# Performance work log

Measured on AMD Instinct MI355X. Metric: run time of the kernel, lower is better.

The kernel has to match this reference:

```python
import jax, jax.numpy as jnp
import numpy as np

N, NFEAT, NHID, NCLASS, NHEADS = 4096, 512, 64, 128, 8
ALPHA = 0.2
NEG = -9e15


def leaky(x):
    return jnp.where(x > 0, x, ALPHA * x)


def setup_inputs() -> dict:
    key = jax.random.key(0)
    k = jax.random.split(key, 6)
    x = jax.random.normal(k[0], (N, NFEAT), dtype=jnp.float32)
    adj = jax.random.randint(k[1], (N, N), 0, 2, dtype=jnp.int32)
    # per-head params (xavier-ish scale)
    W = jax.random.normal(k[2], (NHEADS, NFEAT, NHID), dtype=jnp.float32) * (1.414 * (2.0 / (NFEAT + NHID)) ** 0.5)
    a = jax.random.normal(k[3], (NHEADS, 2 * NHID), dtype=jnp.float32) * (1.414 * (2.0 / (2 * NHID + 1)) ** 0.5)
    W_out = jax.random.normal(k[4], (NHEADS * NHID, NCLASS), dtype=jnp.float32) * (1.414 * (2.0 / (NHEADS * NHID + NCLASS)) ** 0.5)
    a_out = jax.random.normal(k[5], (2 * NCLASS,), dtype=jnp.float32) * (1.414 * (2.0 / (2 * NCLASS + 1)) ** 0.5)
    return {"x": x, "adj": adj, "W": W, "a": a, "W_out": W_out, "a_out": a_out}


def _gat_layer_multihead(x, adj_mask, W, a):
    # x: [N,F_in], W: [H,F_in,F_out], a: [H,2*F_out]
    h = jnp.einsum('nf,hfo->hno', x, W)           # [H,N,F_out]
    Fo = W.shape[-1]
    a1, a2 = a[:, :Fo], a[:, Fo:]                  # [H,F_out] each
    fi = jnp.einsum('hno,ho->hn', h, a1)           # score contribution of node i
    fj = jnp.einsum('hno,ho->hn', h, a2)
    e = leaky(fi[:, :, None] + fj[:, None, :])     # [H,N,N] == leakyrelu(a . [h_i||h_j])
    e = jnp.where(adj_mask[None], e, NEG)
    att = jax.nn.softmax(e, axis=-1)
    return jnp.einsum('hij,hjo->hio', att, h)      # [H,N,F_out]


def reference(x, adj, W, a, W_out, a_out):
    adj_mask = adj > 0
    # multi-head hidden layer, concat heads (dropout is identity in eval mode)
    hp = _gat_layer_multihead(x, adj_mask, W, a)            # [H,N,NHID]
    xcat = jnp.transpose(hp, (1, 0, 2)).reshape(N, NHEADS * NHID)
    # output attention layer (single head)
    out = _gat_layer_multihead(xcat, adj_mask, W_out[None], a_out[None])[0]  # [N,NCLASS]
    out = jax.nn.elu(out)
    return jax.nn.log_softmax(out, axis=1)
```

## Files before the change

kernel.cpp:

```cpp
#include <hip/hip_runtime.h>
#include <hip/hip_bf16.h>

#define NNODE 4096

typedef __attribute__((ext_vector_type(8))) short bf16x8;
typedef __attribute__((ext_vector_type(4))) float f32x4;
typedef __attribute__((ext_vector_type(8))) unsigned short us8;

__device__ __forceinline__ unsigned short f2bf(float x) {
  __hip_bfloat16 b = __float2bfloat16(x);
  return __builtin_bit_cast(unsigned short, b);
}

__global__ __launch_bounds__(256) void packadj(
    const int* __restrict__ adj, unsigned long long* __restrict__ mask) {
  size_t wid = (size_t)blockIdx.x * 4 + (threadIdx.x >> 6);
  int v = adj[wid * 64 + (threadIdx.x & 63)];
  unsigned long long b = __ballot(v != 0);
  if ((threadIdx.x & 63) == 0) mask[wid] = b;
}

__global__ __launch_bounds__(256) void transpose_bf16(
    const float* __restrict__ src, short* __restrict__ dst, int Nr, int Fsrc) {
  __shared__ float tile[64][68];
  const int t  = threadIdx.x;
  const int n0 = blockIdx.x * 64, o0 = blockIdx.y * 64;
  const int h  = blockIdx.z;
  const float* S = src + ((size_t)h * Nr + n0) * Fsrc + o0;
  short* D = dst + ((size_t)h * Fsrc + o0) * Nr + n0;
  const int r = t >> 2, cs = (t & 3) * 16;
  #pragma unroll
  for (int k2 = 0; k2 < 4; ++k2) {
    float4 v = *(const float4*)&S[(size_t)r * Fsrc + cs + k2 * 4];
    *(float4*)&tile[r][cs + k2 * 4] = v;
  }
  __syncthreads();
  const int o = t >> 2, ns = (t & 3) * 16;
  us8 u0, u1;
  #pragma unroll
  for (int e = 0; e < 8; ++e) u0[e] = f2bf(tile[ns + e][o]);
  #pragma unroll
  for (int e = 0; e < 8; ++e) u1[e] = f2bf(tile[ns + 8 + e][o]);
  *(us8*)&D[(size_t)o * Nr + ns]     = u0;
  *(us8*)&D[(size_t)o * Nr + ns + 8] = u1;
}

__global__ __launch_bounds__(256) void gemm_mfma(
    const float* __restrict__ A, const short* __restrict__ Wt,
    float* __restrict__ C, int M, int K, int Nfull) {
  __shared__ short As[64][72];
  const int t  = threadIdx.x;
  const int lane = t & 63;
  const int w  = t >> 6;
  const int i0 = blockIdx.x * 64;
  const int c0 = blockIdx.y * 64;
  const int h  = blockIdx.z;
  const short* Bh = Wt + ((size_t)h * Nfull + c0) * K;
  float*       Ch = C + (size_t)h * M * Nfull;

  const int R0 = (w >> 1) * 32;
  const int C0 = (w & 1) * 32;
  const int lr = lane & 15;
  const int lk = lane >> 4;

  const int arow = t >> 2;
  const int aseg = (t & 3) * 16;

  f32x4 acc[2][2] = {};

  const short* b00p = &Bh[(size_t)(C0 + lr) * K + lk * 8];
  const short* b10p = &Bh[(size_t)(C0 + 16 + lr) * K + lk * 8];

  bf16x8 bc[4];
  bc[0] = *(const bf16x8*)(b00p);
  bc[1] = *(const bf16x8*)(b10p);
  bc[2] = *(const bf16x8*)(b00p + 32);
  bc[3] = *(const bf16x8*)(b10p + 32);

  for (int k0 = 0; k0 < K; k0 += 64) {
    {
      const float* src = &A[(size_t)(i0 + arow) * K + k0 + aseg];
      float4 v0 = *(const float4*)(src);
      float4 v1 = *(const float4*)(src + 4);
      float4 v2 = *(const float4*)(src + 8);
      float4 v3 = *(const float4*)(src + 12);
      us8 u0, u1;
      u0[0] = f2bf(v0.x); u0[1] = f2bf(v0.y); u0[2] = f2bf(v0.z); u0[3] = f2bf(v0.w);
      u0[4] = f2bf(v1.x); u0[5] = f2bf(v1.y); u0[6] = f2bf(v1.z); u0[7] = f2bf(v1.w);
      u1[0] = f2bf(v2.x); u1[1] = f2bf(v2.y); u1[2] = f2bf(v2.z); u1[3] = f2bf(v2.w);
      u1[4] = f2bf(v3.x); u1[5] = f2bf(v3.y); u1[6] = f2bf(v3.z); u1[7] = f2bf(v3.w);
      *(us8*)&As[arow][aseg]     = u0;
      *(us8*)&As[arow][aseg + 8] = u1;
    }
    bf16x8 bn[4];
    {
      int kn = (k0 + 64 < K) ? (k0 + 64) : k0;
      bn[0] = *(const bf16x8*)(b00p + kn);
      bn[1] = *(const bf16x8*)(b10p + kn);
      bn[2] = *(const bf16x8*)(b00p + kn + 32);
      bn[3] = *(const bf16x8*)(b10p + kn + 32);
    }
    __syncthreads();
    #pragma unroll
    for (int kc = 0; kc < 64; kc += 32) {
      bf16x8 a0 = *(const bf16x8*)&As[R0 + lr][kc + lk * 8];
      bf16x8 a1 = *(const bf16x8*)&As[R0 + 16 + lr][kc + lk * 8];
      bf16x8 b0 = bc[(kc >> 5) * 2 + 0];
      bf16x8 b1 = bc[(kc >> 5) * 2 + 1];
      acc[0][0] = __builtin_amdgcn_mfma_f32_16x16x32_bf16(a0, b0, acc[0][0], 0, 0, 0);
      acc[0][1] = __builtin_amdgcn_mfma_f32_16x16x32_bf16(a0, b1, acc[0][1], 0, 0, 0);
      acc[1][0] = __builtin_amdgcn_mfma_f32_16x16x32_bf16(a1, b0, acc[1][0], 0, 0, 0);
      acc[1][1] = __builtin_amdgcn_mfma_f32_16x16x32_bf16(a1, b1, acc[1][1], 0, 0, 0);
    }
    bc[0] = bn[0]; bc[1] = bn[1]; bc[2] = bn[2]; bc[3] = bn[3];
    __syncthreads();
  }

  #pragma unroll
  for (int fa = 0; fa < 2; ++fa) {
    #pragma unroll
    for (int fb = 0; fb < 2; ++fb) {
      #pragma unroll
      for (int reg = 0; reg < 4; ++reg) {
        int row = R0 + fa * 16 + lk * 4 + reg;
        int col = C0 + fb * 16 + lr;
        Ch[(size_t)(i0 + row) * Nfull + c0 + col] = acc[fa][fb][reg];
      }
    }
  }
}

template<int F>
__global__ __launch_bounds__(256) void wa_kernel(
    const float* __restrict__ W, const float* __restrict__ a,
    float* __restrict__ wa) {
  const int gid  = blockIdx.x * 4 + (threadIdx.x >> 6);
  const int lane = threadIdx.x & 63;
  const int h = gid >> 9;
  const int k = gid & 511;
  const float* wrow = W + ((size_t)h * 512 + k) * F;
  const float* ah = a + h * 2 * F;
  float v1 = 0.f, v2 = 0.f;
  #pragma unroll
  for (int o = lane; o < F; o += 64) {
    float wv = wrow[o];
    v1 += wv * ah[o];
    v2 += wv * ah[F + o];
  }
  #pragma unroll
  for (int off = 32; off; off >>= 1) {
    v1 += __shfl_xor(v1, off);
    v2 += __shfl_xor(v2, off);
  }
  if (lane == 0) {
    wa[((size_t)h * 2 + 0) * 512 + k] = v1;
    wa[((size_t)h * 2 + 1) * 512 + k] = v2;
  }
}

template<int NH>
__global__ __launch_bounds__(256) void fidot_kernel(
    const float* __restrict__ X, const float* __restrict__ wa,
    float* __restrict__ fi, float* __restrict__ fj,
    float* __restrict__ eiP, float* __restrict__ eiN,
    float* __restrict__ ejP, float* __restrict__ ejN) {
  const int gid  = blockIdx.x * 4 + (threadIdx.x >> 6);
  const int lane = threadIdx.x & 63;
  const int h = gid >> 12;
  const int n = gid & 4095;
  const float* xr = X + (size_t)n * 512;
  const float* w1 = wa + (size_t)h * 2 * 512;
  const float* w2 = w1 + 512;
  float v1 = 0.f, v2 = 0.f;
  #pragma unroll
  for (int it = 0; it < 8; ++it) {
    int k = lane + it * 64;
    float xv = xr[k];
    v1 += xv * w1[k];
    v2 += xv * w2[k];
  }
  #pragma unroll
  for (int off = 32; off; off >>= 1) {
    v1 += __shfl_xor(v1, off);
    v2 += __shfl_xor(v2, off);
  }
  if (lane == 0) {
    int idx = h * NNODE + n;
    fi[idx] = v1;
    fj[idx] = v2;
    eiP[idx] = __expf(v1);
    eiN[idx] = __expf(0.2f * v1);
    ejP[idx] = __expf(v2);
    ejN[idx] = __expf(0.2f * v2);
  }
}

template<int OT, int JLEN>
__global__ __launch_bounds__(256) void pv_split(
    const short* __restrict__ hT, const float* __restrict__ fi,
    const float* __restrict__ eiP, const float* __restrict__ eiN,
    const float* __restrict__ fj, const float* __restrict__ ejP,
    const float* __restrict__ ejN, const unsigned long long* __restrict__ mask,
    float* __restrict__ pnum, float* __restrict__ pl, int Fh) {
  __shared__ short pT[64][72];
  __shared__ short hTl[OT][64][72];
  __shared__ float fjL[64], ejPL[64], ejNL[64];
  __shared__ float lred[64][4];

  const int t      = threadIdx.x;
  const int lane   = t & 63;
  const int w      = t >> 6;
  const int i0     = blockIdx.x * 64;
  const int chunk  = blockIdx.y;
  const int nchunk = gridDim.y;
  const int h      = blockIdx.z;
  const int hN     = h * NNODE;
  const short* hTs = hT + (size_t)h * Fh * NNODE;

  const int R0 = (w >> 1) * 32;
  const int C0 = (w & 1) * 32;
  const int lr = lane & 15;
  const int lk = lane >> 4;

  const int ar = t >> 2;
  const int jc = (t & 3) * 16;
  const float thr  = -fi[hN + i0 + ar];
  const float eiPr = eiP[hN + i0 + ar];
  const float eiNr = eiN[hN + i0 + ar];
  const unsigned short* mrow =
      (const unsigned short*)mask + (size_t)(i0 + ar) * (NNODE / 16);

  f32x4 acc[OT][2][2] = {};
  float lsum = 0.0f;

  const int jbase = chunk * JLEN;
  for (int jt = 0; jt < JLEN; jt += 64) {
    const int j0 = jbase + jt;
    {
      const int o = t >> 2, seg = t & 3;
      #pragma unroll
      for (int ot = 0; ot < OT; ++ot) {
        const short* src = hTs + (size_t)(ot * 64 + o) * NNODE + j0 + seg * 16;
        float4 v0 = *(const float4*)(src);
        float4 v1 = *(const float4*)(src + 8);
        *(float4*)&hTl[ot][o][seg * 16]     = v0;
        *(float4*)&hTl[ot][o][seg * 16 + 8] = v1;
      }
    }
    if (t < 64) {
      fjL[t]  = fj[hN + j0 + t];
      ejPL[t] = ejP[hN + j0 + t];
      ejNL[t] = ejN[hN + j0 + t];
    }
    __syncthreads();

    {
      unsigned int mb = mrow[(j0 + jc) >> 4];
      unsigned short pk[16];
      #pragma unroll
      for (int g = 0; g < 4; ++g) {
        float4 f4 = *(const float4*)&fjL[jc + g * 4];
        float4 eP = *(const float4*)&ejPL[jc + g * 4];
        float4 eN = *(const float4*)&ejNL[jc + g * 4];
        float p0 = (f4.x > thr) ? eiPr * eP.x : eiNr * eN.x;
        float p1 = (f4.y > thr) ? eiPr * eP.y : eiNr * eN.y;
        float p2 = (f4.z > thr) ? eiPr * eP.z : eiNr * eN.z;
        float p3 = (f4.w > thr) ? eiPr * eP.w : eiNr * eN.w;
        p0 = (mb & (1u << (4 * g + 0))) ? p0 : 0.f;
        p1 = (mb & (1u << (4 * g + 1))) ? p1 : 0.f;
        p2 = (mb & (1u << (4 * g + 2))) ? p2 : 0.f;
        p3 = (mb & (1u << (4 * g + 3))) ? p3 : 0.f;
        lsum += p0 + p1 + p2 + p3;
        pk[4 * g + 0] = f2bf(p0); pk[4 * g + 1] = f2bf(p1);
        pk[4 * g + 2] = f2bf(p2); pk[4 * g + 3] = f2bf(p3);
      }
      *(us8*)&pT[ar][jc]     = *(const us8*)&pk[0];
      *(us8*)&pT[ar][jc + 8] = *(const us8*)&pk[8];
    }
    __syncthreads();

    #pragma unroll
    for (int kc = 0; kc < 64; kc += 32) {
      bf16x8 a0 = *(const bf16x8*)&pT[R0 + lr][kc + lk * 8];
      bf16x8 a1 = *(const bf16x8*)&pT[R0 + 16 + lr][kc + lk * 8];
      #pragma unroll
      for (int ot = 0; ot < OT; ++ot) {
        bf16x8 b0 = *(const bf16x8*)&hTl[ot][C0 + lr][kc + lk * 8];
        bf16x8 b1 = *(const bf16x8*)&hTl[ot][C0 + 16 + lr][kc + lk * 8];
        acc[ot][0][0] = __builtin_amdgcn_mfma_f32_16x16x32_bf16(a0, b0, acc[ot][0][0], 0, 0, 0);
        acc[ot][0][1] = __builtin_amdgcn_mfma_f32_16x16x32_bf16(a0, b1, acc[ot][0][1], 0, 0, 0);
        acc[ot][1][0] = __builtin_amdgcn_mfma_f32_16x16x32_bf16(a1, b0, acc[ot][1][0], 0, 0, 0);
        acc[ot][1][1] = __builtin_amdgcn_mfma_f32_16x16x32_bf16(a1, b1, acc[ot][1][1], 0, 0, 0);
      }
    }
    __syncthreads();
  }

  lred[ar][t & 3] = lsum;
  __syncthreads();
  if (t < 64)
    pl[(size_t)(h * nchunk + chunk) * NNODE + i0 + t] =
        lred[t][0] + lred[t][1] + lred[t][2] + lred[t][3];

  float* pout = pnum + ((size_t)(h * nchunk + chunk) * NNODE + i0) * (OT * 64);
  #pragma unroll
  for (int ot = 0; ot < OT; ++ot) {
    #pragma unroll
    for (int fa = 0; fa < 2; ++fa) {
      #pragma unroll
      for (int fb = 0; fb < 2; ++fb) {
        #pragma unroll
        for (int reg = 0; reg < 4; ++reg) {
          int row = R0 + fa * 16 + lk * 4 + reg;
          int col = ot * 64 + C0 + fb * 16 + lr;
          pout[(size_t)row * (OT * 64) + col] = acc[ot][fa][fb][reg];
        }
      }
    }
  }
}

template<int NC>
__global__ __launch_bounds__(256) void combine1(
    const float* __restrict__ pnum, const float* __restrict__ pl,
    float* __restrict__ xcat) {
  const int n = blockIdx.x, t = threadIdx.x;
  #pragma unroll
  for (int rep = 0; rep < 2; ++rep) {
    int col = t + rep * 256;
    int h = col >> 6, o = col & 63;
    float s = 0.f, L = 0.f;
    #pragma unroll
    for (int c = 0; c < NC; ++c) {
      s += pnum[((size_t)(h * NC + c) * NNODE + n) * 64 + o];
      L += pl[(size_t)(h * NC + c) * NNODE + n];
    }
    xcat[(size_t)n * 512 + col] = s / L;
  }
}

__global__ __launch_bounds__(128) void combine2_final(
    const float* __restrict__ pnum, const float* __restrict__ pl,
    float* __restrict__ dout) {
  const int n = blockIdx.x, t = threadIdx.x;
  float s = 0.f, L = 0.f;
  #pragma unroll
  for (int c = 0; c < 8; ++c) {
    s += pnum[((size_t)c * NNODE + n) * 128 + t];
    L += pl[(size_t)c * NNODE + n];
  }
  float v = s / L;
  float e = v > 0.f ? v : (__expf(v) - 1.0f);
  float mx = e;
  #pragma unroll
  for (int off = 32; off; off >>= 1) mx = fmaxf(mx, __shfl_xor(mx, off));
  __shared__ float r2[2];
  if ((t & 63) == 0) r2[t >> 6] = mx;
  __syncthreads();
  mx = fmaxf(r2[0], r2[1]);
  float sm = __expf(e - mx);
  #pragma unroll
  for (int off = 32; off; off >>= 1) sm += __shfl_xor(sm, off);
  __shared__ float s2[2];
  if ((t & 63) == 0) s2[t >> 6] = sm;
  __syncthreads();
  float sum = s2[0] + s2[1];
  dout[(size_t)n * 128 + t] = e - mx - __logf(sum);
}

extern "C" void kernel_launch(void* const* d_in, const int* in_sizes, int n_in,
                              void* d_out, int out_size, void* d_ws, size_t ws_size,
                              hipStream_t stream) {
  const float* x     = (const float*)d_in[0];
  const int*   adj   = (const int*)d_in[1];
  const float* W     = (const float*)d_in[2];
  const float* a     = (const float*)d_in[3];
  const float* W_out = (const float*)d_in[4];
  const float* a_out = (const float*)d_in[5];
  float* out = (float*)d_out;

  float* ws = (float*)d_ws;
  unsigned long long* mask = (unsigned long long*)ws;
  float* hbuf = ws + 524288;
  float* xcat = hbuf + 2097152;
  short* hT   = (short*)(xcat + 2097152);
  float* pnum = (float*)(((short*)hT) + 2097152);
  float* pl   = pnum + 4194304;
  short* Wt1  = (short*)(pl + 131072);
  short* Wt2  = Wt1 + 262144;
  float* fi1  = (float*)(Wt2 + 65536);
  float* fj1  = fi1 + 32768;
  float* eiP1 = fj1 + 32768;
  float* eiN1 = eiP1 + 32768;
  float* ejP1 = eiN1 + 32768;
  float* ejN1 = ejP1 + 32768;
  float* fi2  = ejN1 + 32768;
  float* fj2  = fi2 + 4096;
  float* eiP2 = fj2 + 4096;
  float* eiN2 = eiP2 + 4096;
  float* ejP2 = eiN2 + 4096;
  float* ejN2 = ejP2 + 4096;
  float* wa1  = ejN2 + 4096;
  float* wa2  = wa1 + 8192;

  packadj<<<dim3(NNODE * NNODE / 64 / 4), 256, 0, stream>>>(adj, mask);
  transpose_bf16<<<dim3(8, 1, 8), 256, 0, stream>>>(W, Wt1, 512, 64);
  transpose_bf16<<<dim3(8, 2, 1), 256, 0, stream>>>(W_out, Wt2, 512, 128);
  wa_kernel<64><<<dim3(8 * 512 / 4), 256, 0, stream>>>(W, a, wa1);
  wa_kernel<128><<<dim3(512 / 4), 256, 0, stream>>>(W_out, a_out, wa2);

  gemm_mfma<<<dim3(64, 1, 8), 256, 0, stream>>>(x, Wt1, hbuf, 4096, 512, 64);
  transpose_bf16<<<dim3(64, 1, 8), 256, 0, stream>>>(hbuf, hT, 4096, 64);
  fidot_kernel<8><<<dim3(8 * 4096 / 4), 256, 0, stream>>>(x, wa1, fi1, fj1, eiP1, eiN1, ejP1, ejN1);
  pv_split<1, 2048><<<dim3(64, 2, 8), 256, 0, stream>>>(hT, fi1, eiP1, eiN1, fj1, ejP1, ejN1, mask, pnum, pl, 64);
  combine1<2><<<dim3(NNODE), 256, 0, stream>>>(pnum, pl, xcat);

  gemm_mfma<<<dim3(64, 2, 1), 256, 0, stream>>>(xcat, Wt2, hbuf, 4096, 512, 128);
  transpose_bf16<<<dim3(64, 2, 1), 256, 0, stream>>>(hbuf, hT, 4096, 128);
  fidot_kernel<1><<<dim3(4096 / 4), 256, 0, stream>>>(xcat, wa2, fi2, fj2, eiP2, eiN2, ejP2, ejN2);
  pv_split<2, 512><<<dim3(64, 8, 1), 256, 0, stream>>>(hT, fi2, eiP2, eiN2, fj2, ejP2, ejN2, mask, pnum, pl, 128);
  combine2_final<<<dim3(NNODE), 128, 0, stream>>>(pnum, pl, out);
}
```

Measured before the change: 273.2 us.

## Fuse transposes into GEMM epilogue, register-resident P in attention, fuse fidot into combine

The GEMM now writes its output directly as transposed bf16, which removes the separate fp32 hbuf and the transpose kernels. The pv_split kernel builds the attention-probability A-fragment in registers, with each wave owning 16 rows. This drops the pT shared-memory staging and one barrier per tile. fidot for layer 1 handles all 8 heads per node with weights staged in LDS, and the layer-2 fidot is fused into combine1, saving launches and rereads of x/xcat. In exchange there are higher register counts, an uncoalesced 4-element transposed store in the GEMM epilogue, and 32KB of LDS per block in fidot8.

```diff
diff --git a/kernel.cpp b/kernel.cpp
--- a/kernel.cpp
+++ b/kernel.cpp
@@ -5,6 +5,7 @@
 
 typedef __attribute__((ext_vector_type(8))) short bf16x8;
 typedef __attribute__((ext_vector_type(4))) float f32x4;
+typedef __attribute__((ext_vector_type(4))) unsigned short us4;
 typedef __attribute__((ext_vector_type(8))) unsigned short us8;
 
 __device__ __forceinline__ unsigned short f2bf(float x) {
@@ -47,7 +48,7 @@
 
 __global__ __launch_bounds__(256) void gemm_mfma(
     const float* __restrict__ A, const short* __restrict__ Wt,
-    float* __restrict__ C, int M, int K, int Nfull) {
+    short* __restrict__ hTout, int M, int K, int Nfull) {
   __shared__ short As[64][72];
   const int t  = threadIdx.x;
   const int lane = t & 63;
@@ -56,7 +57,7 @@
   const int c0 = blockIdx.y * 64;
   const int h  = blockIdx.z;
   const short* Bh = Wt + ((size_t)h * Nfull + c0) * K;
-  float*       Ch = C + (size_t)h * M * Nfull;
+  short*       Hh = hTout + (size_t)h * Nfull * M;
 
   const int R0 = (w >> 1) * 32;
   const int C0 = (w & 1) * 32;
@@ -120,12 +121,12 @@
   for (int fa = 0; fa < 2; ++fa) {
     #pragma unroll
     for (int fb = 0; fb < 2; ++fb) {
+      int col  = c0 + C0 + fb * 16 + lr;
+      int rowb = i0 + R0 + fa * 16 + lk * 4;
+      us4 pk;
       #pragma unroll
-      for (int reg = 0; reg < 4; ++reg) {
-        int row = R0 + fa * 16 + lk * 4 + reg;
-        int col = C0 + fb * 16 + lr;
-        Ch[(size_t)(i0 + row) * Nfull + c0 + col] = acc[fa][fb][reg];
-      }
+      for (int reg = 0; reg < 4; ++reg) pk[reg] = f2bf(acc[fa][fb][reg]);
+      *(us4*)&Hh[(size_t)col * M + rowb] = pk;
     }
   }
 }
@@ -158,40 +159,41 @@
   }
 }
 
-template<int NH>
-__global__ __launch_bounds__(256) void fidot_kernel(
+__global__ __launch_bounds__(256) void fidot8(
     const float* __restrict__ X, const float* __restrict__ wa,
     float* __restrict__ fi, float* __restrict__ fj,
     float* __restrict__ eiP, float* __restrict__ eiN,
     float* __restrict__ ejP, float* __restrict__ ejN) {
-  const int gid  = blockIdx.x * 4 + (threadIdx.x >> 6);
+  __shared__ float sw[8192];
+  for (int idx = threadIdx.x; idx < 8192; idx += 256) sw[idx] = wa[idx];
+  __syncthreads();
+  const int n    = blockIdx.x * 4 + (threadIdx.x >> 6);
   const int lane = threadIdx.x & 63;
-  const int h = gid >> 12;
-  const int n = gid & 4095;
   const float* xr = X + (size_t)n * 512;
-  const float* w1 = wa + (size_t)h * 2 * 512;
-  const float* w2 = w1 + 512;
-  float v1 = 0.f, v2 = 0.f;
+  float v[16] = {};
   #pragma unroll
   for (int it = 0; it < 8; ++it) {
     int k = lane + it * 64;
     float xv = xr[k];
-    v1 += xv * w1[k];
-    v2 += xv * w2[k];
-  }
-  #pragma unroll
-  for (int off = 32; off; off >>= 1) {
-    v1 += __shfl_xor(v1, off);
-    v2 += __shfl_xor(v2, off);
-  }
+    #pragma unroll
+    for (int hh = 0; hh < 8; ++hh) {
+      v[2 * hh]     += xv * sw[(2 * hh) * 512 + k];
+      v[2 * hh + 1] += xv * sw[(2 * hh + 1) * 512 + k];
+    }
+  }
+  #pragma unroll
+  for (int off = 32; off; off >>= 1)
+    #pragma unroll
+    for (int i = 0; i < 16; ++i) v[i] += __shfl_xor(v[i], off);
   if (lane == 0) {
-    int idx = h * NNODE + n;
-    fi[idx] = v1;
-    fj[idx] = v2;
-    eiP[idx] = __expf(v1);
-    eiN[idx] = __expf(0.2f * v1);
-    ejP[idx] = __expf(v2);
-    ejN[idx] = __expf(0.2f * v2);
+    #pragma unroll
+    for (int hh = 0; hh < 8; ++hh) {
+      int idx = hh * NNODE + n;
+      float f1 = v[2 * hh], f2 = v[2 * hh + 1];
+      fi[idx] = f1;  fj[idx] = f2;
+      eiP[idx] = __expf(f1); eiN[idx] = __expf(0.2f * f1);
+      ejP[idx] = __expf(f2); ejN[idx] = __expf(0.2f * f2);
+    }
   }
 }
 
@@ -202,10 +204,8 @@
     const float* __restrict__ fj, const float* __restrict__ ejP,
     const float* __restrict__ ejN, const unsigned long long* __restrict__ mask,
     float* __restrict__ pnum, float* __restrict__ pl, int Fh) {
-  __shared__ short pT[64][72];
   __shared__ short hTl[OT][64][72];
   __shared__ float fjL[64], ejPL[64], ejNL[64];
-  __shared__ float lred[64][4];
 
   const int t      = threadIdx.x;
   const int lane   = t & 63;
@@ -217,20 +217,15 @@
   const int hN     = h * NNODE;
   const short* hTs = hT + (size_t)h * Fh * NNODE;
 
-  const int R0 = (w >> 1) * 32;
-  const int C0 = (w & 1) * 32;
   const int lr = lane & 15;
   const int lk = lane >> 4;
-
-  const int ar = t >> 2;
-  const int jc = (t & 3) * 16;
-  const float thr  = -fi[hN + i0 + ar];
-  const float eiPr = eiP[hN + i0 + ar];
-  const float eiNr = eiN[hN + i0 + ar];
-  const unsigned short* mrow =
-      (const unsigned short*)mask + (size_t)(i0 + ar) * (NNODE / 16);
-
-  f32x4 acc[OT][2][2] = {};
+  const int arow = i0 + w * 16 + lr;
+  const float thr  = -fi[hN + arow];
+  const float eiPr = eiP[hN + arow];
+  const float eiNr = eiN[hN + arow];
+  const unsigned long long* mrow = mask + (size_t)arow * (NNODE / 64);
+
+  f32x4 acc[OT][4] = {};
   float lsum = 0.0f;
 
   const int jbase = chunk * JLEN;
@@ -254,88 +249,104 @@
     }
     __syncthreads();
 
-    {
-      unsigned int mb = mrow[(j0 + jc) >> 4];
-      unsigned short pk[16];
+    const unsigned long long mw = mrow[j0 >> 6];
+    #pragma unroll
+    for (int kk = 0; kk < 2; ++kk) {
+      const int kc = kk * 32;
+      const int kb = kc + lk * 8;
+      float4 fj0 = *(const float4*)&fjL[kb];
+      float4 fj1 = *(const float4*)&fjL[kb + 4];
+      float4 eP0 = *(const float4*)&ejPL[kb];
+      float4 eP1 = *(const float4*)&ejPL[kb + 4];
+      float4 eN0 = *(const float4*)&ejNL[kb];
+      float4 eN1 = *(const float4*)&ejNL[kb + 4];
+      const unsigned int mb = (unsigned int)(mw >> kb) & 0xFFu;
+      float pv[8];
+      pv[0] = (fj0.x > thr) ? eiPr * eP0.x : eiNr * eN0.x;
+      pv[1] = (fj0.y > thr) ? eiPr * eP0.y : eiNr * eN0.y;
+      pv[2] = (fj0.z > thr) ? eiPr * eP0.z : eiNr * eN0.z;
+      pv[3] = (fj0.w > thr) ? eiPr * eP0.w : eiNr * eN0.w;
+      pv[4] = (fj1.x > thr) ? eiPr * eP1.x : eiNr * eN1.x;
+      pv[5] = (fj1.y > thr) ? eiPr * eP1.y : eiNr * eN1.y;
+      pv[6] = (fj1.z > thr) ? eiPr * eP1.z : eiNr * eN1.z;
+      pv[7] = (fj1.w > thr) ? eiPr * eP1.w : eiNr * eN1.w;
+      us8 af;
       #pragma unroll
-      for (int g = 0; g < 4; ++g) {
-        float4 f4 = *(const float4*)&fjL[jc + g * 4];
-        float4 eP = *(const float4*)&ejPL[jc + g * 4];
-        float4 eN = *(const float4*)&ejNL[jc + g * 4];
-        float p0 = (f4.x > thr) ? eiPr * eP.x : eiNr * eN.x;
-        float p1 = (f4.y > thr) ? eiPr * eP.y : eiNr * eN.y;
-        float p2 = (f4.z > thr) ? eiPr * eP.z : eiNr * eN.z;
-        float p3 = (f4.w > thr) ? eiPr * eP.w : eiNr * eN.w;
-        p0 = (mb & (1u << (4 * g + 0))) ? p0 : 0.f;
-        p1 = (mb & (1u << (4 * g + 1))) ? p1 : 0.f;
-        p2 = (mb & (1u << (4 * g + 2))) ? p2 : 0.f;
-        p3 = (mb & (1u << (4 * g + 3))) ? p3 : 0.f;
-        lsum += p0 + p1 + p2 + p3;
-        pk[4 * g + 0] = f2bf(p0); pk[4 * g + 1] = f2bf(p1);
-        pk[4 * g + 2] = f2bf(p2); pk[4 * g + 3] = f2bf(p3);
+      for (int e = 0; e < 8; ++e) {
+        float p = (mb & (1u << e)) ? pv[e] : 0.0f;
+        lsum += p;
+        af[e] = f2bf(p);
       }
-      *(us8*)&pT[ar][jc]     = *(const us8*)&pk[0];
-      *(us8*)&pT[ar][jc + 8] = *(const us8*)&pk[8];
-    }
-    __syncthreads();
-
-    #pragma unroll
-    for (int kc = 0; kc < 64; kc += 32) {
-      bf16x8 a0 = *(const bf16x8*)&pT[R0 + lr][kc + lk * 8];
-      bf16x8 a1 = *(const bf16x8*)&pT[R0 + 16 + lr][kc + lk * 8];
+      bf16x8 a = __builtin_bit_cast(bf16x8, af);
       #pragma unroll
       for (int ot = 0; ot < OT; ++ot) {
-        bf16x8 b0 = *(const bf16x8*)&hTl[ot][C0 + lr][kc + lk * 8];
-        bf16x8 b1 = *(const bf16x8*)&hTl[ot][C0 + 16 + lr][kc + lk * 8];
-        acc[ot][0][0] = __builtin_amdgcn_mfma_f32_16x16x32_bf16(a0, b0, acc[ot][0][0], 0, 0, 0);
-        acc[ot][0][1] = __builtin_amdgcn_mfma_f32_16x16x32_bf16(a0, b1, acc[ot][0][1], 0, 0, 0);
-        acc[ot][1][0] = __builtin_amdgcn_mfma_f32_16x16x32_bf16(a1, b0, acc[ot][1][0], 0, 0, 0);
-        acc[ot][1][1] = __builtin_amdgcn_mfma_f32_16x16x32_bf16(a1, b1, acc[ot][1][1], 0, 0, 0);
-      }
-    }
-    __syncthreads();
-  }
-
-  lred[ar][t & 3] = lsum;
-  __syncthreads();
-  if (t < 64)
-    pl[(size_t)(h * nchunk + chunk) * NNODE + i0 + t] =
-        lred[t][0] + lred[t][1] + lred[t][2] + lred[t][3];
-
-  float* pout = pnum + ((size_t)(h * nchunk + chunk) * NNODE + i0) * (OT * 64);
-  #pragma unroll
-  for (int ot = 0; ot < OT; ++ot) {
-    #pragma unroll
-    for (int fa = 0; fa < 2; ++fa) {
-      #pragma unroll
-      for (int fb = 0; fb < 2; ++fb) {
         #pragma unroll
-        for (int reg = 0; reg < 4; ++reg) {
-          int row = R0 + fa * 16 + lk * 4 + reg;
-          int col = ot * 64 + C0 + fb * 16 + lr;
-          pout[(size_t)row * (OT * 64) + col] = acc[ot][fa][fb][reg];
+        for (int c = 0; c < 4; ++c) {
+          bf16x8 b = *(const bf16x8*)&hTl[ot][c * 16 + lr][kb];
+          acc[ot][c] = __builtin_amdgcn_mfma_f32_16x16x32_bf16(a, b, acc[ot][c], 0, 0, 0);
         }
       }
     }
-  }
-}
-
-template<int NC>
-__global__ __launch_bounds__(256) void combine1(
+    __syncthreads();
+  }
+
+  lsum += __shfl_xor(lsum, 16);
+  lsum += __shfl_xor(lsum, 32);
+  if (lk == 0)
+    pl[(size_t)(h * nchunk + chunk) * NNODE + arow] = lsum;
+
+  float* pout = pnum + ((size_t)(h * nchunk + chunk) * NNODE + i0) * (OT * 64);
+  #pragma unroll
+  for (int ot = 0; ot < OT; ++ot) {
+    #pragma unroll
+    for (int c = 0; c < 4; ++c) {
+      #pragma unroll
+      for (int reg = 0; reg < 4; ++reg) {
+        int row = w * 16 + lk * 4 + reg;
+        int col = ot * 64 + c * 16 + lr;
+        pout[(size_t)row * (OT * 64) + col] = acc[ot][c][reg];
+      }
+    }
+  }
+}
+
+__global__ __launch_bounds__(256) void combine1_fidot(
     const float* __restrict__ pnum, const float* __restrict__ pl,
-    float* __restrict__ xcat) {
+    const float* __restrict__ wa2, float* __restrict__ xcat,
+    float* __restrict__ fi2, float* __restrict__ fj2,
+    float* __restrict__ eiP2, float* __restrict__ eiN2,
+    float* __restrict__ ejP2, float* __restrict__ ejN2) {
   const int n = blockIdx.x, t = threadIdx.x;
+  float d1 = 0.f, d2 = 0.f;
   #pragma unroll
   for (int rep = 0; rep < 2; ++rep) {
     int col = t + rep * 256;
     int h = col >> 6, o = col & 63;
     float s = 0.f, L = 0.f;
     #pragma unroll
-    for (int c = 0; c < NC; ++c) {
-      s += pnum[((size_t)(h * NC + c) * NNODE + n) * 64 + o];
-      L += pl[(size_t)(h * NC + c) * NNODE + n];
-    }
-    xcat[(size_t)n * 512 + col] = s / L;
+    for (int c = 0; c < 2; ++c) {
+      s += pnum[((size_t)(h * 2 + c) * NNODE + n) * 64 + o];
+      L += pl[(size_t)(h * 2 + c) * NNODE + n];
+    }
+    float xv = s / L;
+    xcat[(size_t)n * 512 + col] = xv;
+    d1 += xv * wa2[col];
+    d2 += xv * wa2[512 + col];
+  }
+  #pragma unroll
+  for (int off = 32; off; off >>= 1) {
+    d1 += __shfl_xor(d1, off);
+    d2 += __shfl_xor(d2, off);
+  }
+  __shared__ float red[2][4];
+  if ((t & 63) == 0) { red[0][t >> 6] = d1; red[1][t >> 6] = d2; }
+  __syncthreads();
+  if (t == 0) {
+    float f1 = red[0][0] + red[0][1] + red[0][2] + red[0][3];
+    float f2 = red[1][0] + red[1][1] + red[1][2] + red[1][3];
+    fi2[n] = f1;  fj2[n] = f2;
+    eiP2[n] = __expf(f1); eiN2[n] = __expf(0.2f * f1);
+    ejP2[n] = __expf(f2); ejN2[n] = __expf(0.2f * f2);
   }
 }
 
@@ -381,14 +392,15 @@
 
   float* ws = (float*)d_ws;
   unsigned long long* mask = (unsigned long long*)ws;
-  float* hbuf = ws + 524288;
-  float* xcat = hbuf + 2097152;
+  float* xcat = ws + 524288;
   short* hT   = (short*)(xcat + 2097152);
   float* pnum = (float*)(((short*)hT) + 2097152);
   float* pl   = pnum + 4194304;
   short* Wt1  = (short*)(pl + 131072);
   short* Wt2  = Wt1 + 262144;
-  float* fi1  = (float*)(Wt2 + 65536);
+  float* wa1  = (float*)(Wt2 + 65536);
+  float* wa2  = wa1 + 8192;
+  float* fi1  = wa2 + 1024;
   float* fj1  = fi1 + 32768;
   float* eiP1 = fj1 + 32768;
   float* eiN1 = eiP1 + 32768;
@@ -400,8 +412,6 @@
   float* eiN2 = eiP2 + 4096;
   float* ejP2 = eiN2 + 4096;
   float* ejN2 = ejP2 + 4096;
-  float* wa1  = ejN2 + 4096;
-  float* wa2  = wa1 + 8192;
 
   packadj<<<dim3(NNODE * NNODE / 64 / 4), 256, 0, stream>>>(adj, mask);
   transpose_bf16<<<dim3(8, 1, 8), 256, 0, stream>>>(W, Wt1, 512, 64);
@@ -409,15 +419,12 @@
   wa_kernel<64><<<dim3(8 * 512 / 4), 256, 0, stream>>>(W, a, wa1);
   wa_kernel<128><<<dim3(512 / 4), 256, 0, stream>>>(W_out, a_out, wa2);
 
-  gemm_mfma<<<dim3(64, 1, 8), 256, 0, stream>>>(x, Wt1, hbuf, 4096, 512, 64);
-  transpose_bf16<<<dim3(64, 1, 8), 256, 0, stream>>>(hbuf, hT, 4096, 64);
-  fidot_kernel<8><<<dim3(8 * 4096 / 4), 256, 0, stream>>>(x, wa1, fi1, fj1, eiP1, eiN1, ejP1, ejN1);
+  gemm_mfma<<<dim3(64, 1, 8), 256, 0, stream>>>(x, Wt1, hT, 4096, 512, 64);
+  fidot8<<<dim3(4096 / 4), 256, 0, stream>>>(x, wa1, fi1, fj1, eiP1, eiN1, ejP1, ejN1);
   pv_split<1, 2048><<<dim3(64, 2, 8), 256, 0, stream>>>(hT, fi1, eiP1, eiN1, fj1, ejP1, ejN1, mask, pnum, pl, 64);
-  combine1<2><<<dim3(NNODE), 256, 0, stream>>>(pnum, pl, xcat);
-
-  gemm_mfma<<<dim3(64, 2, 1), 256, 0, stream>>>(xcat, Wt2, hbuf, 4096, 512, 128);
-  transpose_bf16<<<dim3(64, 2, 1), 256, 0, stream>>>(hbuf, hT, 4096, 128);
-  fidot_kernel<1><<<dim3(4096 / 4), 256, 0, stream>>>(xcat, wa2, fi2, fj2, eiP2, eiN2, ejP2, ejN2);
+  combine1_fidot<<<dim3(NNODE), 256, 0, stream>>>(pnum, pl, wa2, xcat, fi2, fj2, eiP2, eiN2, ejP2, ejN2);
+
+  gemm_mfma<<<dim3(64, 2, 1), 256, 0, stream>>>(xcat, Wt2, hT, 4096, 512, 128);
   pv_split<2, 512><<<dim3(64, 8, 1), 256, 0, stream>>>(hT, fi2, eiP2, eiN2, fj2, ejP2, ejN2, mask, pnum, pl, 128);
   combine2_final<<<dim3(NNODE), 128, 0, stream>>>(pnum, pl, out);
 }
```

Result: faster. 248.0 us (-9.2%).
